# Performance work log

Measured on AMD Instinct MI355X. Metric: run time of the kernel, lower is better.

Reference implementation:

```python
import jax, jax.numpy as jnp
import numpy as np

B, S, D = 1, 4096, 512      # batch, seq, model dim
E, K, H = 64, 2, 256        # routed experts, top-k, expert hidden (moe_inter_dim)
HS = 2048                   # shared expert hidden = n_shared_experts * inter_dim
EPS = 1e-5                  # LayerNorm eps (torch default)


def setup_inputs() -> dict:
    key = jax.random.key(0)
    ks = jax.random.split(key, 16)
    n = lambda k, shp, s=0.02: jax.random.normal(k, shp, dtype=jnp.float32) * s
    return {
        "x": jax.random.normal(ks[0], (B, S, D), dtype=jnp.float32),
        # gate Linear(dim -> E)
        "Wg": n(ks[1], (E, D)), "bg": n(ks[2], (E,)),
        # per-expert LayerNorm affine
        "gamma": 1.0 + n(ks[3], (E, D)), "beta": n(ks[4], (E, D)),
        # per-expert SwiGLU: w1, w3: D->H ; w2: H->D
        "W1": n(ks[5], (E, D, H)), "b1": n(ks[6], (E, H)),
        "W3": n(ks[7], (E, D, H)), "b3": n(ks[8], (E, H)),
        "W2": n(ks[9], (E, H, D)), "b2": n(ks[10], (E, D)),
        # shared expert (same Expert structure, hidden HS)
        "gs": 1.0 + n(ks[11], (D,)), "bs": n(ks[11], (D,)),
        "Ws1": n(ks[12], (D, HS)), "bs1": n(ks[12], (HS,)),
        "Ws3": n(ks[13], (D, HS)), "bs3": n(ks[13], (HS,)),
        "Ws2": n(ks[14], (HS, D)), "bs2": n(ks[15], (D,)),
    }


def reference(x, Wg, bg, gamma, beta, W1, b1, W3, b3, W2, b2,
              gs, bs, Ws1, bs1, Ws3, bs3, Ws2, bs2):
    shape = x.shape
    xt = x.reshape(-1, D)                      # [T, D] tokens
    T = xt.shape[0]

    # ---- Gate (eval path: sigmoid scores, no load balancing / bias / groups) ----
    scores = jax.nn.sigmoid(xt @ Wg.T + bg)    # [T, E]
    w, idx = jax.lax.top_k(scores, K)          # [T, K]
    w = w / w.sum(-1, keepdims=True)           # sigmoid path normalization; route_scale = 1
    # dense combine weights: cw[t, e] = routing weight of token t on expert e (0 if not routed)
    cw = jnp.zeros((T, E), xt.dtype).at[jnp.arange(T)[:, None], idx].add(w)

    # ---- Shared LayerNorm statistics (affine folded per-expert below) ----
    mu = xt.mean(-1, keepdims=True)
    var = ((xt - mu) ** 2).mean(-1, keepdims=True)
    nx = (xt - mu) * jax.lax.rsqrt(var + EPS)  # [T, D], unit-affine normalized

    # Fold each expert's LN affine (gamma_e, beta_e) into its w1/w3:
    # (nx*g + b) @ W = nx @ (g[:,None]*W) + b @ W
    W1p = gamma[:, :, None] * W1
    b1p = b1 + jnp.einsum('ed,edh->eh', beta, W1)
    W3p = gamma[:, :, None] * W3
    b3p = b3 + jnp.einsum('ed,edh->eh', beta, W3)

    h1 = jnp.einsum('td,edh->eth', nx, W1p) + b1p[:, None, :]   # [E, T, H]
    h3 = jnp.einsum('td,edh->eth', nx, W3p) + b3p[:, None, :]
    h = jax.nn.silu(h1) * h3                                     # SwiGLU, [E, T, H]

    # Weighted combine: y[t] = sum_e cw[t,e] * (h[e,t] @ W2[e] + b2[e])
    hw = h * cw.T[:, :, None]                                    # [E, T, H]
    y = jnp.einsum('eth,ehd->td', hw, W2) + cw @ b2              # [T, D]

    # ---- Shared expert (applied to every token) ----
    nxs = nx * gs + bs
    hs = jax.nn.silu(nxs @ Ws1 + bs1) * (nxs @ Ws3 + bs3)        # [T, HS]
    z = hs @ Ws2 + bs2

    return (y + z).reshape(shape)
```

## Files before the change

kernel.cpp:

```cpp
#include <hip/hip_runtime.h>
#include <math.h>

typedef unsigned short u16;
typedef unsigned int u32;
typedef __attribute__((ext_vector_type(8))) short bf16x8;
typedef __attribute__((ext_vector_type(4))) float f32x4;

#define TT   4096
#define DM   512
#define NE   64
#define HE   256
#define HSH  2048
#define NSH  8
#define PADBASE 16384
#define MAXTILES 384
#define MAXRT    128

#define WAITV(N) asm volatile("s_waitcnt vmcnt(" #N ")" ::: "memory")
#define SBAR()   __builtin_amdgcn_s_barrier()
#define SCHEDB() __builtin_amdgcn_sched_barrier(0)

__device__ __forceinline__ float sig_(float z){ return 1.f/(1.f+__expf(-z)); }

__device__ __forceinline__ u16 f2bf(float x){
  u32 u = __builtin_bit_cast(u32, x);
  u = (u + 0x7FFFu + ((u >> 16) & 1u)) >> 16;
  return (u16)u;
}

__device__ __forceinline__ f32x4 mfma16(bf16x8 a, bf16x8 b, f32x4 c){
  return __builtin_amdgcn_mfma_f32_16x16x32_bf16(a, b, c, 0, 0, 0);
}

__device__ __forceinline__ bf16x8 frd(const char* tile, int row, int csw){
  return *(const bf16x8*)(tile + row*64 + csw);
}

__device__ __forceinline__ void gl16(const void* g, void* l){
  __builtin_amdgcn_global_load_lds(
      (const __attribute__((address_space(1))) unsigned int*)g,
      (__attribute__((address_space(3))) unsigned int*)l, 16, 0, 0);
}

template<int K, int N>
__device__ __forceinline__ void cvt_tile(
    const float* __restrict__ in, const float* __restrict__ scale,
    const float* __restrict__ fvec, u16* __restrict__ out,
    float* __restrict__ fout, int local, int tid, char* LT)
{
  const int nbk = K >> 6;
  const int nbn = N >> 8;
  const int pm = nbk * nbn;
  const int z = local / pm, rem = local - z*pm;
  const int kt = rem % nbk, ntile = rem / nbk;
  const int k0 = kt*64;
  const int n  = ntile*256 + tid;

  const float* src = in + (size_t)z*K*N + (size_t)k0*N + n;
  const float* scp = scale ? (scale + (size_t)z*K + k0) : nullptr;
  const float* fvp = fvec  ? (fvec  + (size_t)z*K + k0) : nullptr;

  float fsum = 0.f;
  #pragma unroll 4
  for (int kk = 0; kk < 8; kk++){
    float v[8];
    #pragma unroll
    for (int j = 0; j < 8; j++) v[j] = src[(size_t)(kk*8 + j)*N];
    u16 b[8];
    if (scp){
      #pragma unroll
      for (int j = 0; j < 8; j++) b[j] = f2bf(v[j]*scp[kk*8 + j]);
    } else {
      #pragma unroll
      for (int j = 0; j < 8; j++) b[j] = f2bf(v[j]);
    }
    if (fvp){
      #pragma unroll
      for (int j = 0; j < 8; j++) fsum += v[j]*fvp[kk*8 + j];
    }
    uint4 pk;
    pk.x = (u32)b[0] | ((u32)b[1] << 16);
    pk.y = (u32)b[2] | ((u32)b[3] << 16);
    pk.z = (u32)b[4] | ((u32)b[5] << 16);
    pk.w = (u32)b[6] | ((u32)b[7] << 16);
    *(uint4*)(LT + tid*144 + kk*16) = pk;
  }
  if (fout) atomicAdd(fout + (size_t)z*N + n, fsum);
  __syncthreads();

  u16* obase = out + (size_t)z*K*N + (size_t)(ntile*256)*K + k0;
  #pragma unroll 2
  for (int cc = 0; cc < 8; cc++){
    const int g = cc*256 + tid;
    const int row = g >> 3, ch = g & 7;
    uint4 v = *(const uint4*)(LT + row*144 + ch*16);
    *(uint4*)(obase + (size_t)row*K + ch*8) = v;
  }
}

__global__ __launch_bounds__(256) void k_pre(
    const float* __restrict__ W1, const float* __restrict__ W3,
    const float* __restrict__ W2, const float* __restrict__ Ws1,
    const float* __restrict__ Ws3, const float* __restrict__ Ws2,
    const float* __restrict__ gamma, const float* __restrict__ beta,
    const float* __restrict__ gs, const float* __restrict__ bsv,
    u16* __restrict__ W1bT, u16* __restrict__ W3bT, u16* __restrict__ W2bT,
    u16* __restrict__ Ws1bT, u16* __restrict__ Ws3bT, u16* __restrict__ Ws2bT,
    float* __restrict__ b1f, float* __restrict__ b3f,
    const float* __restrict__ x, const float* __restrict__ Wg,
    const float* __restrict__ bg,
    u16* __restrict__ nxb, int* __restrict__ top_idx, float* __restrict__ top_w)
{
  __shared__ __align__(16) char LT[256*144];
  const int bid = blockIdx.x;
  const int tid = threadIdx.x;

  if (bid < 1728){
    if      (bid < 512)  cvt_tile<DM,HE> (W1,  gamma,   beta,    W1bT,  b1f,        bid,      tid, LT);
    else if (bid < 1024) cvt_tile<DM,HE> (W3,  gamma,   beta,    W3bT,  b3f,        bid-512,  tid, LT);
    else if (bid < 1536) cvt_tile<HE,DM> (W2,  nullptr, nullptr, W2bT,  nullptr,    bid-1024, tid, LT);
    else if (bid < 1600) cvt_tile<DM,HSH>(Ws1, gs,      bsv,     Ws1bT, b1f+NE*HE,  bid-1536, tid, LT);
    else if (bid < 1664) cvt_tile<DM,HSH>(Ws3, gs,      bsv,     Ws3bT, b3f+NE*HE,  bid-1600, tid, LT);
    else                 cvt_tile<HSH,DM>(Ws2, nullptr, nullptr, Ws2bT, nullptr,    bid-1664, tid, LT);
    return;
  }

  __shared__ float xs[DM];
  __shared__ float sred[4], ssred[4];
  __shared__ float sc[NE];
  const int t = bid - 1728;

  float2 v = reinterpret_cast<const float2*>(x + (size_t)t*DM)[tid];
  xs[2*tid]   = v.x;
  xs[2*tid+1] = v.y;
  float s  = v.x + v.y;
  float ss = v.x*v.x + v.y*v.y;
  #pragma unroll
  for (int o = 32; o > 0; o >>= 1){ s += __shfl_xor(s, o); ss += __shfl_xor(ss, o); }
  const int wid = tid >> 6, lane = tid & 63;
  if (lane == 0){ sred[wid] = s; ssred[wid] = ss; }
  __syncthreads();
  const float tot = sred[0]+sred[1]+sred[2]+sred[3];
  const float tss = ssred[0]+ssred[1]+ssred[2]+ssred[3];
  const float mu  = tot * (1.f/DM);
  const float var = tss * (1.f/DM) - mu*mu;
  const float rstd = rsqrtf(var + 1e-5f);
  u32 pk = (u32)f2bf((v.x-mu)*rstd) | ((u32)f2bf((v.y-mu)*rstd) << 16);
  *(u32*)(nxb + (size_t)t*DM + 2*tid) = pk;

  const int e = tid >> 2, sub = tid & 3;
  const float4* wrow4 = reinterpret_cast<const float4*>(Wg + (size_t)e*DM);
  const float4* xs4   = reinterpret_cast<const float4*>(xs);
  float acc = 0.f;
  #pragma unroll 4
  for (int i = sub; i < DM/4; i += 4){
    const float4 w = wrow4[i]; const float4 xv = xs4[i];
    acc += xv.x*w.x + xv.y*w.y + xv.z*w.z + xv.w*w.w;
  }
  acc += __shfl_xor(acc, 1);
  acc += __shfl_xor(acc, 2);
  if (sub == 0) sc[e] = acc + bg[e];
  __syncthreads();

  if (tid < 64) {
    const float s0 = sc[tid];
    float m = s0; int mi = tid;
    #pragma unroll
    for (int o = 1; o < 64; o <<= 1){
      float om = __shfl_xor(m, o); int oi = __shfl_xor(mi, o);
      if (om > m || (om == m && oi < mi)) { m = om; mi = oi; }
    }
    float s1 = (tid == mi) ? -INFINITY : s0;
    float m2 = s1; int mi2 = tid;
    #pragma unroll
    for (int o = 1; o < 64; o <<= 1){
      float om = __shfl_xor(m2, o); int oi = __shfl_xor(mi2, o);
      if (om > m2 || (om == m2 && oi < mi2)) { m2 = om; mi2 = oi; }
    }
    if (tid == 0){
      const float w0 = sig_(m), w1 = sig_(m2);
      const float inv = 1.f/(w0+w1);
      top_idx[2*t]   = mi;
      top_idx[2*t+1] = mi2;
      top_w[2*t]     = w0*inv;
      top_w[2*t+1]   = w1*inv;
    }
  }
}

__global__ __launch_bounds__(256) void k_route(
    const int* __restrict__ top_idx, const float* __restrict__ top_w,
    int* __restrict__ bucket_tok, float* __restrict__ bucket_w,
    int* __restrict__ tiles, int* __restrict__ n_tiles)
{
  __shared__ int cnt[NE], base_[NE];
  __shared__ int nroute;
  const int tid = threadIdx.x;
  if (tid < NE) cnt[tid] = 0;
  __syncthreads();
  for (int p = tid; p < TT*2; p += 256) atomicAdd(&cnt[top_idx[p]], 1);
  __syncthreads();
  if (tid == 0){
    int run = 0, ntl = 0;
    for (int e = 0; e < NE; e++){
      base_[e] = run;
      const int c = cnt[e];
      for (int b = 0; b < c; b += 128){
        const int n = (c - b < 128) ? (c - b) : 128;
        tiles[ntl++] = (e << 17) | (((run + b) >> 7) << 8) | n;
      }
      run += ((c + 127) >> 7) << 7;
    }
    nroute = ntl;
    n_tiles[0] = ntl + NSH*(TT/128);
    n_tiles[1] = ntl;
  }
  __syncthreads();
  if (tid < NSH*(TT/128)){
    const int s = tid >> 5, t = tid & 31;
    const int b0 = PADBASE + s*TT + t*128;
    tiles[nroute + tid] = ((NE + s) << 17) | ((b0 >> 7) << 8) | 128;
  }
  if (tid < NE) cnt[tid] = 0;
  __syncthreads();
  for (int p = tid; p < TT*2; p += 256){
    const int e = top_idx[p];
    const int pos = base_[e] + atomicAdd(&cnt[e], 1);
    bucket_tok[pos] = p >> 1;
    bucket_w[pos]   = top_w[p];
  }
}

__global__ __launch_bounds__(512) void k_up(
    const u16* __restrict__ nxb,
    const u16* __restrict__ W1bT, const u16* __restrict__ W3bT,
    const u16* __restrict__ Ws1bT, const u16* __restrict__ Ws3bT,
    const float* __restrict__ b1, const float* __restrict__ b3,
    const float* __restrict__ bs1, const float* __restrict__ bs3,
    const float* __restrict__ b1f, const float* __restrict__ b3f,
    const int* __restrict__ bucket_tok, const float* __restrict__ bucket_w,
    const int* __restrict__ tiles, const int* __restrict__ n_tiles,
    u16* __restrict__ hrout, u16* __restrict__ hs)
{
  if ((int)blockIdx.x >= n_tiles[0]) return;
  const int info = tiles[blockIdx.x];
  const int e  = info >> 17;
  const int b0 = ((info >> 8) & 0x1FF) << 7;
  const int nt = info & 255;
  const bool sh = (e >= NE);
  const int y  = blockIdx.y;

  __shared__ __align__(16) char Ab[2][8192];
  __shared__ __align__(16) char B1b[2][8192];
  __shared__ __align__(16) char B3b[2][8192];
  __shared__ int   toks[128];
  __shared__ float tw[128];

  const int tid = threadIdx.x, wid = tid >> 6, lane = tid & 63;
  const int l15 = lane & 15, q = lane >> 4;

  if (tid < 128){
    int tk; float w;
    if (!sh){
      if (tid < nt){ tk = bucket_tok[b0+tid]; w = bucket_w[b0+tid]; }
      else         { tk = 0; w = 0.f; }
    } else {
      tk = ((b0 - PADBASE) & (TT-1)) + tid; w = 1.f;
    }
    toks[tid] = tk; tw[tid] = w;
  }
  __syncthreads();

  const u16* w1e = sh ? (Ws1bT + (size_t)(e-NE)*HE*DM) : (W1bT + (size_t)e*HE*DM);
  const u16* w3e = sh ? (Ws3bT + (size_t)(e-NE)*HE*DM) : (W3bT + (size_t)e*HE*DM);

  const int srow = lane >> 2;
  const int csrc = (((lane & 3) ^ ((lane >> 3) & 3))) * 8;
  const u16* asrc = nxb + (size_t)toks[wid*16 + srow]*DM + csrc;
  const u16* b1s  = w1e + (size_t)(y*128 + wid*16 + srow)*DM + csrc;
  const u16* b3s  = w3e + (size_t)(y*128 + wid*16 + srow)*DM + csrc;
  const int loff = wid*1024;

#define UP_STAGE(ph, k0) do{ \
    gl16(asrc + (k0), Ab[ph] + loff); \
    gl16(b1s  + (k0), B1b[ph] + loff); \
    gl16(b3s  + (k0), B3b[ph] + loff); \
  } while(0)

  const int wm = (wid & 1)*64, wn = (wid >> 1)*32;

  const float* ob1 = sh ? (bs1 + (size_t)(e-NE)*HE) : (b1 + (size_t)e*HE);
  const float* ob3 = sh ? (bs3 + (size_t)(e-NE)*HE) : (b3 + (size_t)e*HE);
  f32x4 acc1[4][2], acc3[4][2];
  #pragma unroll
  for (int fn = 0; fn < 2; fn++){
    const int h = y*128 + wn + fn*16 + l15;
    const float v1 = ob1[h] + b1f[(size_t)e*HE + h];
    const float v3 = ob3[h] + b3f[(size_t)e*HE + h];
    #pragma unroll
    for (int fm = 0; fm < 4; fm++){
      acc1[fm][fn] = (f32x4){v1,v1,v1,v1};
      acc3[fm][fn] = (f32x4){v3,v3,v3,v3};
    }
  }

  UP_STAGE(0, 0);
  const int csw = (q ^ ((l15 >> 1) & 3)) * 16;

  for (int ks = 0; ks < DM/32; ks++){
    const int cur = ks & 1;
    if (ks + 1 < DM/32){ UP_STAGE(cur^1, (ks+1)*32); WAITV(3); }
    else               { WAITV(0); }
    SBAR();
    __builtin_amdgcn_s_setprio(1);
    const char* A  = Ab[cur];
    const char* B1 = B1b[cur];
    const char* B3 = B3b[cur];
    bf16x8 fa[4];
    #pragma unroll
    for (int fm = 0; fm < 4; fm++) fa[fm] = frd(A, wm + fm*16 + l15, csw);
    #pragma unroll
    for (int fn = 0; fn < 2; fn++){
      bf16x8 fb1 = frd(B1, wn + fn*16 + l15, csw);
      bf16x8 fb3 = frd(B3, wn + fn*16 + l15, csw);
      #pragma unroll
      for (int fm = 0; fm < 4; fm++){
        acc1[fm][fn] = mfma16(fa[fm], fb1, acc1[fm][fn]);
        acc3[fm][fn] = mfma16(fa[fm], fb3, acc3[fm][fn]);
      }
    }
    __builtin_amdgcn_s_setprio(0);
    SCHEDB();
    SBAR();
  }
#undef UP_STAGE

  const int tbase = sh ? ((b0 - PADBASE) & (TT-1)) : 0;
  const int scol  = sh ? (e - NE)*HE : 0;
  #pragma unroll
  for (int fm = 0; fm < 4; fm++){
    #pragma unroll
    for (int fn = 0; fn < 2; fn++){
      const int hl = y*128 + wn + fn*16 + l15;
      #pragma unroll
      for (int r = 0; r < 4; r++){
        const int m = wm + fm*16 + 4*q + r;
        float v = 0.f;
        if (m < nt){
          const float a1 = acc1[fm][fn][r];
          const float a3 = acc3[fm][fn][r];
          v = a1 * sig_(a1) * a3 * tw[m];
        }
        if (sh) hs[(size_t)(tbase+m)*HSH + scol + hl] = f2bf(v);
        else    hrout[(size_t)(b0+m)*HE + hl] = f2bf(v);
      }
    }
  }
}

__global__ __launch_bounds__(512) void k_down(
    const u16* __restrict__ hs, const u16* __restrict__ Ws2bT,
    const float* __restrict__ bs2,
    const u16* __restrict__ hrout, const u16* __restrict__ W2bT,
    const float* __restrict__ b2,
    const int* __restrict__ bucket_tok, const float* __restrict__ bucket_w,
    const int* __restrict__ tiles, const int* __restrict__ n_tiles,
    float* __restrict__ out)
{
  __shared__ __align__(16) char LDS[49152];
  __shared__ int   toks[128];
  __shared__ float tw[128];

  const int tid = threadIdx.x, wid = tid >> 6, lane = tid & 63;
  const int l15 = lane & 15, q = lane >> 4;
  const int csw  = (q ^ ((l15 >> 1) & 3)) * 16;
  const int srow = tid >> 2;
  const int csrc = ((tid & 3) ^ ((tid >> 3) & 3)) * 8;
  const int loff = wid*1024;

  if ((int)blockIdx.x < 512){
    const int kc = blockIdx.x & 3;
    const int d0 = ((blockIdx.x >> 2) & 3) * 128;
    const int t0 = (blockIdx.x >> 4) * 128;
    char* Ab = LDS;
    char* Bb = LDS + 16384;

    const u16* asrc = hs    + (size_t)(t0 + srow)*HSH + kc*512 + csrc;
    const u16* bsrc = Ws2bT + (size_t)(d0 + srow)*HSH + kc*512 + csrc;

#define DS_STAGE(ph, k0) do{ \
    gl16(asrc + (k0), Ab + (ph)*8192 + loff); \
    gl16(bsrc + (k0), Bb + (ph)*8192 + loff); \
  } while(0)

    const int wm = (wid & 1)*64, wn = (wid >> 1)*32;

    f32x4 acc[4][2];
    #pragma unroll
    for (int fm = 0; fm < 4; fm++)
      #pragma unroll
      for (int fn = 0; fn < 2; fn++) acc[fm][fn] = (f32x4){0.f,0.f,0.f,0.f};

    DS_STAGE(0, 0);

    for (int ks = 0; ks < 16; ks++){
      const int cur = ks & 1;
      if (ks + 1 < 16){ DS_STAGE(cur^1, (ks+1)*32); WAITV(2); }
      else            { WAITV(0); }
      SBAR();
      __builtin_amdgcn_s_setprio(1);
      const char* A = Ab + cur*8192;
      const char* B = Bb + cur*8192;
      bf16x8 fa[4];
      #pragma unroll
      for (int fm = 0; fm < 4; fm++) fa[fm] = frd(A, wm + fm*16 + l15, csw);
      #pragma unroll
      for (int fn = 0; fn < 2; fn++){
        bf16x8 fb = frd(B, wn + fn*16 + l15, csw);
        #pragma unroll
        for (int fm = 0; fm < 4; fm++)
          acc[fm][fn] = mfma16(fa[fm], fb, acc[fm][fn]);
      }
      __builtin_amdgcn_s_setprio(0);
      SCHEDB();
      SBAR();
    }
#undef DS_STAGE

    #pragma unroll
    for (int fm = 0; fm < 4; fm++){
      #pragma unroll
      for (int fn = 0; fn < 2; fn++){
        const int d = d0 + wn + fn*16 + l15;
        const float bv = (kc == 0) ? bs2[d] : 0.f;
        #pragma unroll
        for (int r = 0; r < 4; r++){
          const int t = t0 + wm + fm*16 + 4*q + r;
          atomicAdd(out + (size_t)t*DM + d, acc[fm][fn][r] + bv);
        }
      }
    }
    return;
  }

  const int rb = (int)blockIdx.x - 512;
  const int ti = rb >> 1;
  if (ti >= n_tiles[1]) return;
  const int info = tiles[ti];
  const int e  = info >> 17;
  const int b0 = ((info >> 8) & 0x1FF) << 7;
  const int nt = info & 255;
  const int d0 = (rb & 1) * 256;

  char* Ab = LDS;
  char* Bb = LDS + 16384;

  if (tid < 128){
    if (tid < nt){ toks[tid] = bucket_tok[b0+tid]; tw[tid] = bucket_w[b0+tid]; }
    else         { toks[tid] = 0; tw[tid] = 0.f; }
  }
  __syncthreads();

  const u16* w2e = W2bT + (size_t)e*DM*HE;
  const u16* asrc  = hrout + (size_t)(b0 + srow)*HE + csrc;
  const u16* bsrc0 = w2e + (size_t)(d0 + srow)*HE + csrc;
  const u16* bsrc1 = w2e + (size_t)(d0 + 128 + srow)*HE + csrc;

#define DR_STAGE(ph, k0) do{ \
    gl16(asrc  + (k0), Ab + (ph)*8192  + loff); \
    gl16(bsrc0 + (k0), Bb + (ph)*16384 + loff); \
    gl16(bsrc1 + (k0), Bb + (ph)*16384 + 8192 + loff); \
  } while(0)

  const int wm = (wid & 1)*64, wn = (wid >> 1)*64;

  f32x4 acc[4][4];
  #pragma unroll
  for (int fm = 0; fm < 4; fm++)
    #pragma unroll
    for (int fn = 0; fn < 4; fn++) acc[fm][fn] = (f32x4){0.f,0.f,0.f,0.f};

  DR_STAGE(0, 0);

  for (int ks = 0; ks < HE/32; ks++){
    const int cur = ks & 1;
    if (ks + 1 < HE/32){ DR_STAGE(cur^1, (ks+1)*32); WAITV(3); }
    else               { WAITV(0); }
    SBAR();
    __builtin_amdgcn_s_setprio(1);
    const char* A = Ab + cur*8192;
    const char* B = Bb + cur*16384;
    bf16x8 fa[4];
    #pragma unroll
    for (int fm = 0; fm < 4; fm++) fa[fm] = frd(A, wm + fm*16 + l15, csw);
    #pragma unroll
    for (int fn = 0; fn < 4; fn++){
      bf16x8 fb = frd(B, wn + fn*16 + l15, csw);
      #pragma unroll
      for (int fm = 0; fm < 4; fm++)
        acc[fm][fn] = mfma16(fa[fm], fb, acc[fm][fn]);
    }
    __builtin_amdgcn_s_setprio(0);
    SCHEDB();
    SBAR();
  }
#undef DR_STAGE

  #pragma unroll
  for (int fm = 0; fm < 4; fm++){
    #pragma unroll
    for (int fn = 0; fn < 4; fn++){
      const int d = d0 + wn + fn*16 + l15;
      #pragma unroll
      for (int r = 0; r < 4; r++){
        const int m = wm + fm*16 + 4*q + r;
        if (m < nt)
          atomicAdd(out + (size_t)toks[m]*DM + d, acc[fm][fn][r] + tw[m]*b2[(size_t)e*DM + d]);
      }
    }
  }
}

extern "C" void kernel_launch(void* const* d_in, const int* in_sizes, int n_in,
                              void* d_out, int out_size, void* d_ws, size_t ws_size,
                              hipStream_t stream)
{
  (void)in_sizes; (void)n_in; (void)ws_size;
  const float* x     = (const float*)d_in[0];
  const float* Wg    = (const float*)d_in[1];
  const float* bg    = (const float*)d_in[2];
  const float* gamma = (const float*)d_in[3];
  const float* beta  = (const float*)d_in[4];
  const float* W1    = (const float*)d_in[5];
  const float* b1    = (const float*)d_in[6];
  const float* W3    = (const float*)d_in[7];
  const float* b3    = (const float*)d_in[8];
  const float* W2    = (const float*)d_in[9];
  const float* b2    = (const float*)d_in[10];
  const float* gs    = (const float*)d_in[11];
  const float* bs    = (const float*)d_in[12];
  const float* Ws1   = (const float*)d_in[13];
  const float* bs1   = (const float*)d_in[14];
  const float* Ws3   = (const float*)d_in[15];
  const float* bs3   = (const float*)d_in[16];
  const float* Ws2   = (const float*)d_in[17];
  const float* bs2   = (const float*)d_in[18];
  float* out = (float*)d_out;

  char* ws = (char*)d_ws;
  size_t off = 0;
  auto alloc = [&](size_t bytes) -> char* {
    char* p = ws + off;
    off += (bytes + 255) & ~(size_t)255;
    return p;
  };
  u16*   nxb        = (u16*)  alloc((size_t)TT*DM*2);
  int*   top_idx    = (int*)  alloc((size_t)TT*2*4);
  float* top_w      = (float*)alloc((size_t)TT*2*4);
  int*   bucket_tok = (int*)  alloc((size_t)PADBASE*4);
  float* bucket_w   = (float*)alloc((size_t)PADBASE*4);
  int*   tiles      = (int*)  alloc(MAXTILES*4);
  int*   n_tiles    = (int*)  alloc(64);
  u16*   hrout      = (u16*)  alloc((size_t)PADBASE*HE*2);
  u16*   hs         = (u16*)  alloc((size_t)TT*HSH*2);
  u16*   W1bT       = (u16*)  alloc((size_t)NE*HE*DM*2);
  u16*   W3bT       = (u16*)  alloc((size_t)NE*HE*DM*2);
  u16*   W2bT       = (u16*)  alloc((size_t)NE*DM*HE*2);
  u16*   Ws1bT      = (u16*)  alloc((size_t)HSH*DM*2);
  u16*   Ws3bT      = (u16*)  alloc((size_t)HSH*DM*2);
  u16*   Ws2bT      = (u16*)  alloc((size_t)DM*HSH*2);
  float* b1f        = (float*)alloc((size_t)(NE*HE + HSH)*4);
  float* b3f        = (float*)alloc((size_t)(NE*HE + HSH)*4);

  hipMemsetAsync(b1f, 0, (size_t)(NE*HE + HSH)*4, stream);
  hipMemsetAsync(b3f, 0, (size_t)(NE*HE + HSH)*4, stream);
  hipMemsetAsync(out, 0, (size_t)out_size*sizeof(float), stream);

  k_pre<<<dim3(1728 + TT), 256, 0, stream>>>(
      W1, W3, W2, Ws1, Ws3, Ws2, gamma, beta, gs, bs,
      W1bT, W3bT, W2bT, Ws1bT, Ws3bT, Ws2bT, b1f, b3f,
      x, Wg, bg, nxb, top_idx, top_w);

  k_route<<<dim3(1), 256, 0, stream>>>(top_idx, top_w, bucket_tok, bucket_w, tiles, n_tiles);

  k_up<<<dim3(MAXTILES, 2), 512, 0, stream>>>(nxb, W1bT, W3bT, Ws1bT, Ws3bT,
                                              b1, b3, bs1, bs3, b1f, b3f,
                                              bucket_tok, bucket_w, tiles, n_tiles, hrout, hs);
  k_down<<<dim3(768), 512, 0, stream>>>(hs, Ws2bT, bs2, hrout, W2bT, b2,
                                        bucket_tok, bucket_w, tiles, n_tiles, out);
}
```

Measured before the change: 202.0 us.

## Vectorize weight conversion, restructure GEMM pipelines, unify down-projection tiling

The weight-conversion pass now loads float4 vectors, which widens global reads, and writes to a swizzled LDS transpose buffer to reduce bank conflicts. A compile-time flag removes the fold branch where it is not needed. The up and down GEMM loops now wait for all loads and use one barrier per K-step, issuing the next stage's loads after that barrier instead of keeping loads in flight across two barriers. The shared-expert down projection moves to 256-wide N tiles on the same code path as the routed experts, which cuts its block count and increases output-tile reuse. The trade-off is less load/compute overlap per step and more accumulator registers for the shared path.

```diff
diff --git a/kernel.cpp b/kernel.cpp
--- a/kernel.cpp
+++ b/kernel.cpp
@@ -14,7 +14,6 @@
 #define NSH  8
 #define PADBASE 16384
 #define MAXTILES 384
-#define MAXRT    128
 
 #define WAITV(N) asm volatile("s_waitcnt vmcnt(" #N ")" ::: "memory")
 #define SBAR()   __builtin_amdgcn_s_barrier()
@@ -42,7 +41,7 @@
       (__attribute__((address_space(3))) unsigned int*)l, 16, 0, 0);
 }
 
-template<int K, int N>
+template<int K, int N, bool FOLD>
 __device__ __forceinline__ void cvt_tile(
     const float* __restrict__ in, const float* __restrict__ scale,
     const float* __restrict__ fvec, u16* __restrict__ out,
@@ -54,38 +53,47 @@
   const int z = local / pm, rem = local - z*pm;
   const int kt = rem % nbk, ntile = rem / nbk;
   const int k0 = kt*64;
-  const int n  = ntile*256 + tid;
-
-  const float* src = in + (size_t)z*K*N + (size_t)k0*N + n;
-  const float* scp = scale ? (scale + (size_t)z*K + k0) : nullptr;
-  const float* fvp = fvec  ? (fvec  + (size_t)z*K + k0) : nullptr;
-
-  float fsum = 0.f;
-  #pragma unroll 4
-  for (int kk = 0; kk < 8; kk++){
-    float v[8];
-    #pragma unroll
-    for (int j = 0; j < 8; j++) v[j] = src[(size_t)(kk*8 + j)*N];
-    u16 b[8];
-    if (scp){
-      #pragma unroll
-      for (int j = 0; j < 8; j++) b[j] = f2bf(v[j]*scp[kk*8 + j]);
+  const int q = tid >> 6;
+  const int t = tid & 63;
+  const int nb = t*4;
+
+  const float* src = in + (size_t)z*K*N + (size_t)(k0 + q*16)*N + ntile*256 + nb;
+  const float* scp = scale ? (scale + (size_t)z*K + k0 + q*16) : nullptr;
+  const float* fvp = fvec  ? (fvec  + (size_t)z*K + k0 + q*16) : nullptr;
+
+  u32 pk[4][8];
+  float fs0=0.f, fs1=0.f, fs2=0.f, fs3=0.f;
+  #pragma unroll
+  for (int j = 0; j < 16; j++){
+    float4 v = *(const float4*)(src + (size_t)j*N);
+    const float sc = scp ? scp[j] : 1.0f;
+    const u32 b0 = f2bf(v.x*sc), b1 = f2bf(v.y*sc);
+    const u32 b2 = f2bf(v.z*sc), b3 = f2bf(v.w*sc);
+    if (j & 1){
+      pk[0][j>>1] |= b0 << 16; pk[1][j>>1] |= b1 << 16;
+      pk[2][j>>1] |= b2 << 16; pk[3][j>>1] |= b3 << 16;
     } else {
-      #pragma unroll
-      for (int j = 0; j < 8; j++) b[j] = f2bf(v[j]);
-    }
-    if (fvp){
-      #pragma unroll
-      for (int j = 0; j < 8; j++) fsum += v[j]*fvp[kk*8 + j];
-    }
-    uint4 pk;
-    pk.x = (u32)b[0] | ((u32)b[1] << 16);
-    pk.y = (u32)b[2] | ((u32)b[3] << 16);
-    pk.z = (u32)b[4] | ((u32)b[5] << 16);
-    pk.w = (u32)b[6] | ((u32)b[7] << 16);
-    *(uint4*)(LT + tid*144 + kk*16) = pk;
-  }
-  if (fout) atomicAdd(fout + (size_t)z*N + n, fsum);
+      pk[0][j>>1] = b0; pk[1][j>>1] = b1;
+      pk[2][j>>1] = b2; pk[3][j>>1] = b3;
+    }
+    if (FOLD){
+      const float fv = fvp[j];
+      fs0 += v.x*fv; fs1 += v.y*fv; fs2 += v.z*fv; fs3 += v.w*fv;
+    }
+  }
+  #pragma unroll
+  for (int i = 0; i < 4; i++){
+    const int n = nb + i;
+    char* rowp = LT + n*144;
+    const int x = (n >> 3) & 7;
+    *(uint4*)(rowp + (((2*q)  ^x))*16) = *(const uint4*)&pk[i][0];
+    *(uint4*)(rowp + (((2*q+1)^x))*16) = *(const uint4*)&pk[i][4];
+  }
+  if (FOLD){
+    float* fb = fout + (size_t)z*N + ntile*256 + nb;
+    atomicAdd(fb+0, fs0); atomicAdd(fb+1, fs1);
+    atomicAdd(fb+2, fs2); atomicAdd(fb+3, fs3);
+  }
   __syncthreads();
 
   u16* obase = out + (size_t)z*K*N + (size_t)(ntile*256)*K + k0;
@@ -93,7 +101,7 @@
   for (int cc = 0; cc < 8; cc++){
     const int g = cc*256 + tid;
     const int row = g >> 3, ch = g & 7;
-    uint4 v = *(const uint4*)(LT + row*144 + ch*16);
+    uint4 v = *(const uint4*)(LT + row*144 + ((ch ^ ((row>>3)&7))*16));
     *(uint4*)(obase + (size_t)row*K + ch*8) = v;
   }
 }
@@ -116,12 +124,12 @@
   const int tid = threadIdx.x;
 
   if (bid < 1728){
-    if      (bid < 512)  cvt_tile<DM,HE> (W1,  gamma,   beta,    W1bT,  b1f,        bid,      tid, LT);
-    else if (bid < 1024) cvt_tile<DM,HE> (W3,  gamma,   beta,    W3bT,  b3f,        bid-512,  tid, LT);
-    else if (bid < 1536) cvt_tile<HE,DM> (W2,  nullptr, nullptr, W2bT,  nullptr,    bid-1024, tid, LT);
-    else if (bid < 1600) cvt_tile<DM,HSH>(Ws1, gs,      bsv,     Ws1bT, b1f+NE*HE,  bid-1536, tid, LT);
-    else if (bid < 1664) cvt_tile<DM,HSH>(Ws3, gs,      bsv,     Ws3bT, b3f+NE*HE,  bid-1600, tid, LT);
-    else                 cvt_tile<HSH,DM>(Ws2, nullptr, nullptr, Ws2bT, nullptr,    bid-1664, tid, LT);
+    if      (bid < 512)  cvt_tile<DM,HE, true >(W1,  gamma,   beta,    W1bT,  b1f,        bid,      tid, LT);
+    else if (bid < 1024) cvt_tile<DM,HE, true >(W3,  gamma,   beta,    W3bT,  b3f,        bid-512,  tid, LT);
+    else if (bid < 1536) cvt_tile<HE,DM, false>(W2,  nullptr, nullptr, W2bT,  nullptr,    bid-1024, tid, LT);
+    else if (bid < 1600) cvt_tile<DM,HSH,true >(Ws1, gs,      bsv,     Ws1bT, b1f+NE*HE,  bid-1536, tid, LT);
+    else if (bid < 1664) cvt_tile<DM,HSH,true >(Ws3, gs,      bsv,     Ws3bT, b3f+NE*HE,  bid-1600, tid, LT);
+    else                 cvt_tile<HSH,DM,false>(Ws2, nullptr, nullptr, Ws2bT, nullptr,    bid-1664, tid, LT);
     return;
   }
 
@@ -309,13 +317,13 @@
 
   for (int ks = 0; ks < DM/32; ks++){
     const int cur = ks & 1;
-    if (ks + 1 < DM/32){ UP_STAGE(cur^1, (ks+1)*32); WAITV(3); }
-    else               { WAITV(0); }
+    WAITV(0);
     SBAR();
-    __builtin_amdgcn_s_setprio(1);
+    if (ks + 1 < DM/32){ UP_STAGE(cur^1, (ks+1)*32); SCHEDB(); }
     const char* A  = Ab[cur];
     const char* B1 = B1b[cur];
     const char* B3 = B3b[cur];
+    __builtin_amdgcn_s_setprio(1);
     bf16x8 fa[4];
     #pragma unroll
     for (int fm = 0; fm < 4; fm++) fa[fm] = frd(A, wm + fm*16 + l15, csw);
@@ -330,8 +338,6 @@
       }
     }
     __builtin_amdgcn_s_setprio(0);
-    SCHEDB();
-    SBAR();
   }
 #undef UP_STAGE
 
@@ -367,7 +373,8 @@
     const int* __restrict__ tiles, const int* __restrict__ n_tiles,
     float* __restrict__ out)
 {
-  __shared__ __align__(16) char LDS[49152];
+  __shared__ __align__(16) char Ab[2][8192];
+  __shared__ __align__(16) char Bb[2][16384];
   __shared__ int   toks[128];
   __shared__ float tw[128];
 
@@ -377,119 +384,69 @@
   const int srow = tid >> 2;
   const int csrc = ((tid & 3) ^ ((tid >> 3) & 3)) * 8;
   const int loff = wid*1024;
-
-  if ((int)blockIdx.x < 512){
-    const int kc = blockIdx.x & 3;
-    const int d0 = ((blockIdx.x >> 2) & 3) * 128;
-    const int t0 = (blockIdx.x >> 4) * 128;
-    char* Ab = LDS;
-    char* Bb = LDS + 16384;
-
-    const u16* asrc = hs    + (size_t)(t0 + srow)*HSH + kc*512 + csrc;
-    const u16* bsrc = Ws2bT + (size_t)(d0 + srow)*HSH + kc*512 + csrc;
-
-#define DS_STAGE(ph, k0) do{ \
-    gl16(asrc + (k0), Ab + (ph)*8192 + loff); \
-    gl16(bsrc + (k0), Bb + (ph)*8192 + loff); \
+  const int wm = (wid & 1)*64, wn = (wid >> 1)*64;
+
+  const u16* asrc; const u16* bsrc0; const u16* bsrc1;
+  int nsteps, nt, d0;
+  bool shpath;
+  int e = 0, b0 = 0, kc = 0;
+
+  if ((int)blockIdx.x < 256){
+    shpath = true;
+    kc = blockIdx.x & 3;
+    d0 = ((blockIdx.x >> 2) & 1) * 256;
+    const int t0 = (blockIdx.x >> 3) * 128;
+    nsteps = 16; nt = 128;
+    asrc  = hs    + (size_t)(t0 + srow)*HSH + kc*512 + csrc;
+    bsrc0 = Ws2bT + (size_t)(d0 + srow)*HSH + kc*512 + csrc;
+    bsrc1 = Ws2bT + (size_t)(d0 + 128 + srow)*HSH + kc*512 + csrc;
+    if (tid < 128){ toks[tid] = t0 + tid; tw[tid] = 1.f; }
+  } else {
+    shpath = false;
+    const int rb = (int)blockIdx.x - 256;
+    const int ti = rb >> 1;
+    if (ti >= n_tiles[1]) return;
+    const int info = tiles[ti];
+    e  = info >> 17;
+    b0 = ((info >> 8) & 0x1FF) << 7;
+    nt = info & 255;
+    d0 = (rb & 1) * 256;
+    nsteps = 8;
+    const u16* w2e = W2bT + (size_t)e*DM*HE;
+    asrc  = hrout + (size_t)(b0 + srow)*HE + csrc;
+    bsrc0 = w2e + (size_t)(d0 + srow)*HE + csrc;
+    bsrc1 = w2e + (size_t)(d0 + 128 + srow)*HE + csrc;
+    if (tid < 128){
+      if (tid < nt){ toks[tid] = bucket_tok[b0+tid]; tw[tid] = bucket_w[b0+tid]; }
+      else         { toks[tid] = 0; tw[tid] = 0.f; }
+    }
+  }
+  const size_t lda = shpath ? HSH : HE;
+  (void)lda;
+  __syncthreads();
+
+#define DN_STAGE(ph, k0) do{ \
+    gl16(asrc  + (k0), Ab[ph] + loff); \
+    gl16(bsrc0 + (k0), Bb[ph] + loff); \
+    gl16(bsrc1 + (k0), Bb[ph] + 8192 + loff); \
   } while(0)
 
-    const int wm = (wid & 1)*64, wn = (wid >> 1)*32;
-
-    f32x4 acc[4][2];
-    #pragma unroll
-    for (int fm = 0; fm < 4; fm++)
-      #pragma unroll
-      for (int fn = 0; fn < 2; fn++) acc[fm][fn] = (f32x4){0.f,0.f,0.f,0.f};
-
-    DS_STAGE(0, 0);
-
-    for (int ks = 0; ks < 16; ks++){
-      const int cur = ks & 1;
-      if (ks + 1 < 16){ DS_STAGE(cur^1, (ks+1)*32); WAITV(2); }
-      else            { WAITV(0); }
-      SBAR();
-      __builtin_amdgcn_s_setprio(1);
-      const char* A = Ab + cur*8192;
-      const char* B = Bb + cur*8192;
-      bf16x8 fa[4];
-      #pragma unroll
-      for (int fm = 0; fm < 4; fm++) fa[fm] = frd(A, wm + fm*16 + l15, csw);
-      #pragma unroll
-      for (int fn = 0; fn < 2; fn++){
-        bf16x8 fb = frd(B, wn + fn*16 + l15, csw);
-        #pragma unroll
-        for (int fm = 0; fm < 4; fm++)
-          acc[fm][fn] = mfma16(fa[fm], fb, acc[fm][fn]);
-      }
-      __builtin_amdgcn_s_setprio(0);
-      SCHEDB();
-      SBAR();
-    }
-#undef DS_STAGE
-
-    #pragma unroll
-    for (int fm = 0; fm < 4; fm++){
-      #pragma unroll
-      for (int fn = 0; fn < 2; fn++){
-        const int d = d0 + wn + fn*16 + l15;
-        const float bv = (kc == 0) ? bs2[d] : 0.f;
-        #pragma unroll
-        for (int r = 0; r < 4; r++){
-          const int t = t0 + wm + fm*16 + 4*q + r;
-          atomicAdd(out + (size_t)t*DM + d, acc[fm][fn][r] + bv);
-        }
-      }
-    }
-    return;
-  }
-
-  const int rb = (int)blockIdx.x - 512;
-  const int ti = rb >> 1;
-  if (ti >= n_tiles[1]) return;
-  const int info = tiles[ti];
-  const int e  = info >> 17;
-  const int b0 = ((info >> 8) & 0x1FF) << 7;
-  const int nt = info & 255;
-  const int d0 = (rb & 1) * 256;
-
-  char* Ab = LDS;
-  char* Bb = LDS + 16384;
-
-  if (tid < 128){
-    if (tid < nt){ toks[tid] = bucket_tok[b0+tid]; tw[tid] = bucket_w[b0+tid]; }
-    else         { toks[tid] = 0; tw[tid] = 0.f; }
-  }
-  __syncthreads();
-
-  const u16* w2e = W2bT + (size_t)e*DM*HE;
-  const u16* asrc  = hrout + (size_t)(b0 + srow)*HE + csrc;
-  const u16* bsrc0 = w2e + (size_t)(d0 + srow)*HE + csrc;
-  const u16* bsrc1 = w2e + (size_t)(d0 + 128 + srow)*HE + csrc;
-
-#define DR_STAGE(ph, k0) do{ \
-    gl16(asrc  + (k0), Ab + (ph)*8192  + loff); \
-    gl16(bsrc0 + (k0), Bb + (ph)*16384 + loff); \
-    gl16(bsrc1 + (k0), Bb + (ph)*16384 + 8192 + loff); \
-  } while(0)
-
-  const int wm = (wid & 1)*64, wn = (wid >> 1)*64;
-
   f32x4 acc[4][4];
   #pragma unroll
   for (int fm = 0; fm < 4; fm++)
     #pragma unroll
     for (int fn = 0; fn < 4; fn++) acc[fm][fn] = (f32x4){0.f,0.f,0.f,0.f};
 
-  DR_STAGE(0, 0);
-
-  for (int ks = 0; ks < HE/32; ks++){
+  DN_STAGE(0, 0);
+
+  for (int ks = 0; ks < nsteps; ks++){
     const int cur = ks & 1;
-    if (ks + 1 < HE/32){ DR_STAGE(cur^1, (ks+1)*32); WAITV(3); }
-    else               { WAITV(0); }
+    WAITV(0);
     SBAR();
+    if (ks + 1 < nsteps){ DN_STAGE(cur^1, (ks+1)*32); SCHEDB(); }
+    const char* A = Ab[cur];
+    const char* B = Bb[cur];
     __builtin_amdgcn_s_setprio(1);
-    const char* A = Ab + cur*8192;
-    const char* B = Bb + cur*16384;
     bf16x8 fa[4];
     #pragma unroll
     for (int fm = 0; fm < 4; fm++) fa[fm] = frd(A, wm + fm*16 + l15, csw);
@@ -501,21 +458,24 @@
         acc[fm][fn] = mfma16(fa[fm], fb, acc[fm][fn]);
     }
     __builtin_amdgcn_s_setprio(0);
-    SCHEDB();
-    SBAR();
-  }
-#undef DR_STAGE
+  }
+#undef DN_STAGE
 
   #pragma unroll
   for (int fm = 0; fm < 4; fm++){
     #pragma unroll
     for (int fn = 0; fn < 4; fn++){
       const int d = d0 + wn + fn*16 + l15;
+      float badd;
+      if (shpath) badd = (kc == 0) ? bs2[d] : 0.f;
+      else        badd = 0.f;
       #pragma unroll
       for (int r = 0; r < 4; r++){
         const int m = wm + fm*16 + 4*q + r;
-        if (m < nt)
-          atomicAdd(out + (size_t)toks[m]*DM + d, acc[fm][fn][r] + tw[m]*b2[(size_t)e*DM + d]);
+        if (m < nt){
+          const float extra = shpath ? badd : tw[m]*b2[(size_t)e*DM + d];
+          atomicAdd(out + (size_t)toks[m]*DM + d, acc[fm][fn][r] + extra);
+        }
       }
     }
   }
@@ -586,6 +546,6 @@
   k_up<<<dim3(MAXTILES, 2), 512, 0, stream>>>(nxb, W1bT, W3bT, Ws1bT, Ws3bT,
                                               b1, b3, bs1, bs3, b1f, b3f,
                                               bucket_tok, bucket_w, tiles, n_tiles, hrout, hs);
-  k_down<<<dim3(768), 512, 0, stream>>>(hs, Ws2bT, bs2, hrout, W2bT, b2,
+  k_down<<<dim3(512), 512, 0, stream>>>(hs, Ws2bT, bs2, hrout, W2bT, b2,
                                         bucket_tok, bucket_w, tiles, n_tiles, out);
 }
```

Result: no change. 205.1 us (median of 5 runs) (+1.5%).
